# Kernel optimization log

Measured on AMD Instinct MI355X. Metric: run time of the kernel, lower is better.

Reference implementation:

```python
import jax, jax.numpy as jnp
import numpy as np
from jax import lax

BATCH = 8192
HID = 10
IN = 64
STEPS = 512
REVERSE = True


def setup_inputs() -> dict:
    key = jax.random.key(0)
    ks = jax.random.split(key, 9)
    s_in = 1.0 / np.sqrt(HID)
    return {
        "hidden": jax.random.normal(ks[0], (1, BATCH, HID), dtype=jnp.float32),
        "w_ih": jax.random.uniform(ks[1], (3 * HID, IN), jnp.float32, -s_in, s_in),
        "w_hh": jax.random.uniform(ks[2], (3 * HID, HID), jnp.float32, -s_in, s_in),
        "b_ih": jax.random.uniform(ks[3], (3 * HID,), jnp.float32, -s_in, s_in),
        "b_hh": jax.random.uniform(ks[4], (3 * HID,), jnp.float32, -s_in, s_in),
        "l1_w": jax.random.uniform(ks[5], (10, HID), jnp.float32, -s_in, s_in),
        "l1_b": jax.random.uniform(ks[6], (10,), jnp.float32, -s_in, s_in),
        "l2_w": jax.random.uniform(ks[7], (IN, 10), jnp.float32, -s_in, s_in),
        "l2_b": jax.random.uniform(ks[8], (IN,), jnp.float32, -s_in, s_in),
        "step": STEPS,
    }


def _gru_cell(h, x, w_ih, w_hh, b_ih, b_hh):
    # PyTorch GRU gate order: reset, update, new
    gi = x @ w_ih.T + b_ih  # [B, 3H]
    gh = h @ w_hh.T + b_hh  # [B, 3H]
    i_r, i_z, i_n = jnp.split(gi, 3, axis=-1)
    h_r, h_z, h_n = jnp.split(gh, 3, axis=-1)
    r = jax.nn.sigmoid(i_r + h_r)
    z = jax.nn.sigmoid(i_z + h_z)
    n = jnp.tanh(i_n + r * h_n)
    return (1.0 - z) * n + z * h


def reference(hidden, w_ih, w_hh, b_ih, b_hh, l1_w, l1_b, l2_w, l2_b, step):
    h0 = hidden[0]  # [B, H]
    B = h0.shape[0]
    x0 = jnp.zeros((B, IN), dtype=h0.dtype)  # first GRU input is zeros

    def body(carry, _):
        h, x = carry
        h_new = _gru_cell(h, x, w_ih, w_hh, b_ih, b_hh)
        o = h_new @ l1_w.T + l1_b          # l1 on GRU output
        x_next = o @ l2_w.T + l2_b         # l2 feeds next GRU step
        return (h_new, x_next), o

    _, outs = lax.scan(body, (h0, x0), None, length=step)  # [T, B, 10]
    outs = jnp.transpose(outs, (1, 0, 2))  # [B, T, 10]
    if REVERSE:
        outs = outs[:, ::-1, :]
    return outs
```

## Files before the change

### kernel.cpp

```cpp
#include <hip/hip_runtime.h>

#define HID 10
#define STEPS 512

typedef __attribute__((ext_vector_type(2))) float v2f;

template<int F>
static __device__ __forceinline__ float swz(float v) {
    return __int_as_float(__builtin_amdgcn_ds_swizzle(__float_as_int(v), (F << 5) | 0x10));
}

__global__ __launch_bounds__(64, 2) void gru_decoder_kernel(
    const float* __restrict__ hidden, const float* __restrict__ w_ih,
    const float* __restrict__ w_hh, const float* __restrict__ b_ih,
    const float* __restrict__ b_hh, const float* __restrict__ l1_w,
    const float* __restrict__ l1_b, const float* __restrict__ l2_w,
    const float* __restrict__ l2_b, float* __restrict__ out)
{
    __shared__ float sWx[640];
    __shared__ float sbx[64];
    __shared__ float sWgi[300];
    __shared__ float sbgi[30];
    __shared__ float sWhh[300];

    const int lane = threadIdx.x;
    const int f    = lane & 15;
    const int b    = blockIdx.x * 4 + (lane >> 4);
    const bool ok  = (f < HID);
    const int fi   = ok ? f : 0;

    for (int e = lane; e < 640; e += 64) {
        int i = e / 10, j = e - i * 10;
        float acc = 0.f;
        #pragma unroll
        for (int k = 0; k < 10; ++k) acc += l2_w[i * 10 + k] * l1_w[k * 10 + j];
        sWx[e] = acc;
    }
    {
        float acc = l2_b[lane];
        #pragma unroll
        for (int k = 0; k < 10; ++k) acc += l2_w[lane * 10 + k] * l1_b[k];
        sbx[lane] = acc;
    }
    for (int e = lane; e < 300; e += 64) sWhh[e] = w_hh[e];
    __syncthreads();
    for (int e = lane; e < 300; e += 64) {
        int m = e / 10, j = e - m * 10;
        float acc = 0.f;
        for (int k = 0; k < 64; ++k) acc += w_ih[m * 64 + k] * sWx[k * 10 + j];
        sWgi[e] = acc;
    }
    if (lane < 30) {
        float acc = b_ih[lane];
        for (int k = 0; k < 64; ++k) acc += w_ih[lane * 64 + k] * sbx[k];
        sbgi[lane] = acc;
    }
    __syncthreads();

    const float LOG2E = 1.4426950408889634f;
    const float S2    = 2.f * LOG2E;

    v2f wr2[5], wz2[5], wi2[5], wh2[5], wo2[5];
    #pragma unroll
    for (int k2 = 0; k2 < 5; ++k2) {
        int k0 = 2 * k2, k1 = 2 * k2 + 1;
        float r0 = -(sWgi[fi * 10 + k0] + sWhh[fi * 10 + k0]) * LOG2E;
        float r1 = -(sWgi[fi * 10 + k1] + sWhh[fi * 10 + k1]) * LOG2E;
        float z0 = -(sWgi[(10 + fi) * 10 + k0] + sWhh[(10 + fi) * 10 + k0]) * LOG2E;
        float z1 = -(sWgi[(10 + fi) * 10 + k1] + sWhh[(10 + fi) * 10 + k1]) * LOG2E;
        float i0 = sWgi[(20 + fi) * 10 + k0] * S2;
        float i1 = sWgi[(20 + fi) * 10 + k1] * S2;
        float hh0 = sWhh[(20 + fi) * 10 + k0] * S2;
        float hh1 = sWhh[(20 + fi) * 10 + k1] * S2;
        float o0 = l1_w[fi * 10 + k0];
        float o1 = l1_w[fi * 10 + k1];
        wr2[k2] = ok ? v2f{r0, r1}   : v2f{0.f, 0.f};
        wz2[k2] = ok ? v2f{z0, z1}   : v2f{0.f, 0.f};
        wi2[k2] = ok ? v2f{i0, i1}   : v2f{0.f, 0.f};
        wh2[k2] = ok ? v2f{hh0, hh1} : v2f{0.f, 0.f};
        wo2[k2] = ok ? v2f{o0, o1}   : v2f{0.f, 0.f};
    }
    const float br = ok ? -(sbgi[fi] + b_hh[fi]) * LOG2E : 0.f;
    const float bz = ok ? -(sbgi[10 + fi] + b_hh[10 + fi]) * LOG2E : 0.f;
    const float bi = ok ? sbgi[20 + fi] * S2 : 0.f;
    const float bh = ok ? b_hh[20 + fi] * S2 : 0.f;
    const float bo = ok ? l1_b[fi] : 0.f;
    const float br0_ = ok ? -(b_ih[fi] + b_hh[fi]) * LOG2E : 0.f;
    const float bz0_ = ok ? -(b_ih[10 + fi] + b_hh[10 + fi]) * LOG2E : 0.f;
    const float bni0 = ok ? b_ih[20 + fi] * S2 : 0.f;

    float h = ok ? hidden[(size_t)b * HID + f] : 0.f;

    float* pb = out + (size_t)b * (STEPS * HID) + (size_t)(STEPS - 1) * HID + f;

    {
        float ha[10];
        ha[0] = swz<0>(h); ha[1] = swz<1>(h); ha[2] = swz<2>(h);
        ha[3] = swz<3>(h); ha[4] = swz<4>(h); ha[5] = swz<5>(h);
        ha[6] = swz<6>(h); ha[7] = swz<7>(h); ha[8] = swz<8>(h);
        ha[9] = swz<9>(h);
        float pr = 0.f, pz = 0.f, ph = 0.f;
        #pragma unroll
        for (int k = 0; k < 10; ++k) {
            pr += sWhh[fi * 10 + k] * ha[k];
            pz += sWhh[(10 + fi) * 10 + k] * ha[k];
            ph += sWhh[(20 + fi) * 10 + k] * ha[k];
        }
        float vr = br0_ - pr * LOG2E;
        float vz = bz0_ - pz * LOG2E;
        float r = __builtin_amdgcn_rcpf(1.f + __builtin_amdgcn_exp2f(vr));
        float z = __builtin_amdgcn_rcpf(1.f + __builtin_amdgcn_exp2f(vz));
        float y = bni0 + r * (ph * S2 + bh);
        float n = 1.f - 2.f * __builtin_amdgcn_rcpf(1.f + __builtin_amdgcn_exp2f(y));
        h = ok ? (n + z * (h - n)) : 0.f;
    }

    #pragma unroll 1
    for (int t = 1; t < STEPS; ++t) {
        v2f h2[5];
        h2[0] = v2f{swz<0>(h), swz<1>(h)};
        h2[1] = v2f{swz<2>(h), swz<3>(h)};
        h2[2] = v2f{swz<4>(h), swz<5>(h)};
        h2[3] = v2f{swz<6>(h), swz<7>(h)};
        h2[4] = v2f{swz<8>(h), swz<9>(h)};

        v2f ar = {br, 0.f}, az = {bz, 0.f}, ai = {bi, 0.f},
            ah = {bh, 0.f}, ao = {bo, 0.f};
        #pragma unroll
        for (int k2 = 0; k2 < 5; ++k2) {
            ar += wr2[k2] * h2[k2];
            az += wz2[k2] * h2[k2];
            ai += wi2[k2] * h2[k2];
            ah += wh2[k2] * h2[k2];
            ao += wo2[k2] * h2[k2];
        }
        float arx = ar.x + ar.y;
        float azx = az.x + az.y;
        float aix = ai.x + ai.y;
        float ahx = ah.x + ah.y;
        float o   = ao.x + ao.y;

        float r = __builtin_amdgcn_rcpf(1.f + __builtin_amdgcn_exp2f(arx));
        float z = __builtin_amdgcn_rcpf(1.f + __builtin_amdgcn_exp2f(azx));
        float zh  = z * h;
        float omz = 1.f - z;
        float y = __builtin_fmaf(r, ahx, aix);
        float n = __builtin_fmaf(-2.f,
                    __builtin_amdgcn_rcpf(1.f + __builtin_amdgcn_exp2f(y)), 1.f);
        h = __builtin_fmaf(n, omz, zh);

        if (ok) pb[0] = o;
        pb -= HID;
    }

    {
        v2f h2[5];
        h2[0] = v2f{swz<0>(h), swz<1>(h)};
        h2[1] = v2f{swz<2>(h), swz<3>(h)};
        h2[2] = v2f{swz<4>(h), swz<5>(h)};
        h2[3] = v2f{swz<6>(h), swz<7>(h)};
        h2[4] = v2f{swz<8>(h), swz<9>(h)};
        v2f ao = {bo, 0.f};
        #pragma unroll
        for (int k2 = 0; k2 < 5; ++k2) ao += wo2[k2] * h2[k2];
        if (ok) pb[0] = ao.x + ao.y;
    }
}

extern "C" void kernel_launch(void* const* d_in, const int* in_sizes, int n_in,
                              void* d_out, int out_size, void* d_ws, size_t ws_size,
                              hipStream_t stream) {
    (void)in_sizes; (void)n_in; (void)d_ws; (void)ws_size; (void)out_size;
    dim3 grid(2048), block(64);
    gru_decoder_kernel<<<grid, block, 0, stream>>>(
        (const float*)d_in[0], (const float*)d_in[1], (const float*)d_in[2],
        (const float*)d_in[3], (const float*)d_in[4], (const float*)d_in[5],
        (const float*)d_in[6], (const float*)d_in[7], (const float*)d_in[8],
        (float*)d_out);
}
```

Baseline: 295.3 us.

## Replace ds_swizzle broadcasts with DPP row rotates and merge GRU gate reciprocals

The per-step hidden-state broadcast changes from ten ds_swizzle LDS-crossbar ops to fifteen DPP row_ror rotates. The weights are pre-permuted per lane to match each rotation, and the unused slots are zeroed. The z-gate and n-gate sigmoid/tanh are also rewritten algebraically so one reciprocal replaces two, shortening the transcendental chain. In exchange the rotates add more multiply-add work (8 packed pairs instead of 5) and more weight registers, and occupancy is pinned to 2 waves per EU.

```diff
diff --git a/kernel.cpp b/kernel.cpp
--- a/kernel.cpp
+++ b/kernel.cpp
@@ -10,7 +10,18 @@
     return __int_as_float(__builtin_amdgcn_ds_swizzle(__float_as_int(v), (F << 5) | 0x10));
 }
 
-__global__ __launch_bounds__(64, 2) void gru_decoder_kernel(
+template<int J>
+static __device__ __forceinline__ float frot(float v) {
+    return __int_as_float(__builtin_amdgcn_update_dpp(
+        0, __float_as_int(v), 0x120 + J, 0xF, 0xF, true));
+}
+template<int J>
+static __device__ __forceinline__ int irot(int v) {
+    return __builtin_amdgcn_update_dpp(0, v, 0x120 + J, 0xF, 0xF, true);
+}
+
+__attribute__((amdgpu_waves_per_eu(2, 2)))
+__global__ __launch_bounds__(64) void gru_decoder_kernel(
     const float* __restrict__ hidden, const float* __restrict__ w_ih,
     const float* __restrict__ w_hh, const float* __restrict__ b_ih,
     const float* __restrict__ b_hh, const float* __restrict__ l1_w,
@@ -25,7 +36,8 @@
 
     const int lane = threadIdx.x;
     const int f    = lane & 15;
-    const int b    = blockIdx.x * 4 + (lane >> 4);
+    const int g    = lane >> 4;
+    const int b    = blockIdx.x * 4 + g;
     const bool ok  = (f < HID);
     const int fi   = ok ? f : 0;
 
@@ -60,31 +72,44 @@
     const float LOG2E = 1.4426950408889634f;
     const float S2    = 2.f * LOG2E;
 
-    v2f wr2[5], wz2[5], wi2[5], wh2[5], wo2[5];
-    #pragma unroll
-    for (int k2 = 0; k2 < 5; ++k2) {
-        int k0 = 2 * k2, k1 = 2 * k2 + 1;
-        float r0 = -(sWgi[fi * 10 + k0] + sWhh[fi * 10 + k0]) * LOG2E;
-        float r1 = -(sWgi[fi * 10 + k1] + sWhh[fi * 10 + k1]) * LOG2E;
-        float z0 = -(sWgi[(10 + fi) * 10 + k0] + sWhh[(10 + fi) * 10 + k0]) * LOG2E;
-        float z1 = -(sWgi[(10 + fi) * 10 + k1] + sWhh[(10 + fi) * 10 + k1]) * LOG2E;
-        float i0 = sWgi[(20 + fi) * 10 + k0] * S2;
-        float i1 = sWgi[(20 + fi) * 10 + k1] * S2;
-        float hh0 = sWhh[(20 + fi) * 10 + k0] * S2;
-        float hh1 = sWhh[(20 + fi) * 10 + k1] * S2;
-        float o0 = l1_w[fi * 10 + k0];
-        float o1 = l1_w[fi * 10 + k1];
-        wr2[k2] = ok ? v2f{r0, r1}   : v2f{0.f, 0.f};
-        wz2[k2] = ok ? v2f{z0, z1}   : v2f{0.f, 0.f};
-        wi2[k2] = ok ? v2f{i0, i1}   : v2f{0.f, 0.f};
-        wh2[k2] = ok ? v2f{hh0, hh1} : v2f{0.f, 0.f};
-        wo2[k2] = ok ? v2f{o0, o1}   : v2f{0.f, 0.f};
-    }
+    const int s0  = f;
+    const int s1  = irot<1>(f);   const int s2  = irot<2>(f);
+    const int s3  = irot<3>(f);   const int s4  = irot<4>(f);
+    const int s5  = irot<5>(f);   const int s6  = irot<6>(f);
+    const int s7  = irot<7>(f);   const int s8  = irot<8>(f);
+    const int s9  = irot<9>(f);   const int s10 = irot<10>(f);
+    const int s11 = irot<11>(f);  const int s12 = irot<12>(f);
+    const int s13 = irot<13>(f);  const int s14 = irot<14>(f);
+    const int s15 = irot<15>(f);
+
+    auto WGR = [&](int s)->float { int c = (s < 10) ? s : 0;
+        return (ok && s < 10) ? -(sWgi[fi * 10 + c] + sWhh[fi * 10 + c]) * LOG2E : 0.f; };
+    auto WGZ = [&](int s)->float { int c = (s < 10) ? s : 0;
+        return (ok && s < 10) ? -(sWgi[(10 + fi) * 10 + c] + sWhh[(10 + fi) * 10 + c]) * LOG2E : 0.f; };
+    auto WGI = [&](int s)->float { int c = (s < 10) ? s : 0;
+        return (ok && s < 10) ? sWgi[(20 + fi) * 10 + c] * S2 : 0.f; };
+    auto WGH = [&](int s)->float { int c = (s < 10) ? s : 0;
+        return (ok && s < 10) ? sWhh[(20 + fi) * 10 + c] * S2 : 0.f; };
+    auto WGO = [&](int s)->float { int c = (s < 10) ? s : 0;
+        return (ok && s < 10) ? l1_w[fi * 10 + c] : 0.f; };
+
+    #define MKP(m, sa, sb)                                                       \
+        const v2f wrP##m = {WGR(sa), WGR(sb)};                                   \
+        const v2f wzP##m = {WGZ(sa), WGZ(sb)};                                   \
+        const v2f wiP##m = {WGI(sa), WGI(sb)};                                   \
+        const v2f whP##m = {WGH(sa), WGH(sb)};                                   \
+        const v2f woP##m = {WGO(sa), WGO(sb)};
+    MKP(0, s0,  s1)  MKP(1, s2,  s3)  MKP(2, s4,  s5)  MKP(3, s6,  s7)
+    MKP(4, s8,  s9)  MKP(5, s10, s11) MKP(6, s12, s13) MKP(7, s14, s15)
+    #undef MKP
+
     const float br = ok ? -(sbgi[fi] + b_hh[fi]) * LOG2E : 0.f;
     const float bz = ok ? -(sbgi[10 + fi] + b_hh[10 + fi]) * LOG2E : 0.f;
     const float bi = ok ? sbgi[20 + fi] * S2 : 0.f;
     const float bh = ok ? b_hh[20 + fi] * S2 : 0.f;
     const float bo = ok ? l1_b[fi] : 0.f;
+    const v2f BR2 = {br, 0.f}, BZ2 = {bz, 0.f}, BI2 = {bi, 0.f},
+              BH2 = {bh, 0.f}, BO2 = {bo, 0.f};
     const float br0_ = ok ? -(b_ih[fi] + b_hh[fi]) * LOG2E : 0.f;
     const float bz0_ = ok ? -(b_ih[10 + fi] + b_hh[10 + fi]) * LOG2E : 0.f;
     const float bni0 = ok ? b_ih[20 + fi] * S2 : 0.f;
@@ -117,52 +142,77 @@
 
     #pragma unroll 1
     for (int t = 1; t < STEPS; ++t) {
-        v2f h2[5];
-        h2[0] = v2f{swz<0>(h), swz<1>(h)};
-        h2[1] = v2f{swz<2>(h), swz<3>(h)};
-        h2[2] = v2f{swz<4>(h), swz<5>(h)};
-        h2[3] = v2f{swz<6>(h), swz<7>(h)};
-        h2[4] = v2f{swz<8>(h), swz<9>(h)};
-
-        v2f ar = {br, 0.f}, az = {bz, 0.f}, ai = {bi, 0.f},
-            ah = {bh, 0.f}, ao = {bo, 0.f};
-        #pragma unroll
-        for (int k2 = 0; k2 < 5; ++k2) {
-            ar += wr2[k2] * h2[k2];
-            az += wz2[k2] * h2[k2];
-            ai += wi2[k2] * h2[k2];
-            ah += wh2[k2] * h2[k2];
-            ao += wo2[k2] * h2[k2];
-        }
+        float rh1  = frot<1>(h);   float rh2  = frot<2>(h);
+        float rh3  = frot<3>(h);   float rh4  = frot<4>(h);
+        float rh5  = frot<5>(h);   float rh6  = frot<6>(h);
+        float rh7  = frot<7>(h);   float rh8  = frot<8>(h);
+        float rh9  = frot<9>(h);   float rh10 = frot<10>(h);
+        float rh11 = frot<11>(h);  float rh12 = frot<12>(h);
+        float rh13 = frot<13>(h);  float rh14 = frot<14>(h);
+        float rh15 = frot<15>(h);
+        v2f hp0 = {h,    rh1};   v2f hp1 = {rh2,  rh3};
+        v2f hp2 = {rh4,  rh5};   v2f hp3 = {rh6,  rh7};
+        v2f hp4 = {rh8,  rh9};   v2f hp5 = {rh10, rh11};
+        v2f hp6 = {rh12, rh13};  v2f hp7 = {rh14, rh15};
+
+        v2f ar = wrP0 * hp0 + BR2;
+        v2f az = wzP0 * hp0 + BZ2;
+        v2f ai = wiP0 * hp0 + BI2;
+        v2f ah = whP0 * hp0 + BH2;
+        v2f ao = woP0 * hp0 + BO2;
+        ar += wrP1 * hp1; az += wzP1 * hp1; ai += wiP1 * hp1;
+        ah += whP1 * hp1; ao += woP1 * hp1;
+        ar += wrP2 * hp2; az += wzP2 * hp2; ai += wiP2 * hp2;
+        ah += whP2 * hp2; ao += woP2 * hp2;
+        ar += wrP3 * hp3; az += wzP3 * hp3; ai += wiP3 * hp3;
+        ah += whP3 * hp3; ao += woP3 * hp3;
+        ar += wrP4 * hp4; az += wzP4 * hp4; ai += wiP4 * hp4;
+        ah += whP4 * hp4; ao += woP4 * hp4;
+        ar += wrP5 * hp5; az += wzP5 * hp5; ai += wiP5 * hp5;
+        ah += whP5 * hp5; ao += woP5 * hp5;
+        ar += wrP6 * hp6; az += wzP6 * hp6; ai += wiP6 * hp6;
+        ah += whP6 * hp6; ao += woP6 * hp6;
+        ar += wrP7 * hp7; az += wzP7 * hp7; ai += wiP7 * hp7;
+        ah += whP7 * hp7; ao += woP7 * hp7;
+
         float arx = ar.x + ar.y;
         float azx = az.x + az.y;
         float aix = ai.x + ai.y;
         float ahx = ah.x + ah.y;
         float o   = ao.x + ao.y;
 
-        float r = __builtin_amdgcn_rcpf(1.f + __builtin_amdgcn_exp2f(arx));
-        float z = __builtin_amdgcn_rcpf(1.f + __builtin_amdgcn_exp2f(azx));
-        float zh  = z * h;
-        float omz = 1.f - z;
-        float y = __builtin_fmaf(r, ahx, aix);
-        float n = __builtin_fmaf(-2.f,
-                    __builtin_amdgcn_rcpf(1.f + __builtin_amdgcn_exp2f(y)), 1.f);
-        h = __builtin_fmaf(n, omz, zh);
+        float er = __builtin_amdgcn_exp2f(arx);
+        float rr = __builtin_amdgcn_rcpf(1.f + er);
+        float ez = __builtin_amdgcn_exp2f(azx);
+        float y  = __builtin_fmaf(rr, ahx, aix);
+        float en = __builtin_amdgcn_exp2f(y);
+        float pp = en * ez;
+        float u  = pp + (h - ez);
+        float num = __builtin_fmaf(h, en, u);
+        float den = (pp + (en + ez)) + 1.f;
+        h = num * __builtin_amdgcn_rcpf(den);
 
         if (ok) pb[0] = o;
         pb -= HID;
     }
 
     {
-        v2f h2[5];
-        h2[0] = v2f{swz<0>(h), swz<1>(h)};
-        h2[1] = v2f{swz<2>(h), swz<3>(h)};
-        h2[2] = v2f{swz<4>(h), swz<5>(h)};
-        h2[3] = v2f{swz<6>(h), swz<7>(h)};
-        h2[4] = v2f{swz<8>(h), swz<9>(h)};
-        v2f ao = {bo, 0.f};
-        #pragma unroll
-        for (int k2 = 0; k2 < 5; ++k2) ao += wo2[k2] * h2[k2];
+        float rh1  = frot<1>(h);   float rh2  = frot<2>(h);
+        float rh3  = frot<3>(h);   float rh4  = frot<4>(h);
+        float rh5  = frot<5>(h);   float rh6  = frot<6>(h);
+        float rh7  = frot<7>(h);   float rh8  = frot<8>(h);
+        float rh9  = frot<9>(h);   float rh10 = frot<10>(h);
+        float rh11 = frot<11>(h);  float rh12 = frot<12>(h);
+        float rh13 = frot<13>(h);  float rh14 = frot<14>(h);
+        float rh15 = frot<15>(h);
+        v2f ao = woP0 * v2f{h, rh1} + BO2;
+        ao += woP1 * v2f{rh2,  rh3};
+        ao += woP2 * v2f{rh4,  rh5};
+        ao += woP3 * v2f{rh6,  rh7};
+        ao += woP4 * v2f{rh8,  rh9};
+        ao += woP5 * v2f{rh10, rh11};
+        ao += woP6 * v2f{rh12, rh13};
+        ao += woP7 * v2f{rh14, rh15};
         if (ok) pb[0] = ao.x + ao.y;
     }
 }
```

After: 346.4 us. +17.3%, slower.
